# Kernel optimization log

Hardware: AMD Instinct MI355X
Metric: run time of the kernel (lower is better)

Reference implementation:

```python
import jax, jax.numpy as jnp
import numpy as np

B, DIM, H, W = 8, 128, 64, 64
HEADS = 8
NUMS = DIM // HEADS   # 16
OUT = 256

def setup_inputs() -> dict:
    key = jax.random.key(0)
    k1, k2, k3, k4, k5 = jax.random.split(key, 5)
    x = jax.random.normal(k1, (B, DIM, H, W), dtype=jnp.float32)
    # per-group 1x1 conv (num_heads -> 1): weight [nums, heads], bias [nums]
    W1 = jax.random.normal(k2, (NUMS, HEADS), dtype=jnp.float32) * (1.0 / np.sqrt(HEADS))
    b1 = jax.random.normal(k3, (NUMS,), dtype=jnp.float32) * 0.01
    # final 1x1 conv (nums*dim -> out_dim): weight [out, nums*dim], bias [out]
    W2 = jax.random.normal(k4, (OUT, NUMS * DIM), dtype=jnp.float32) * (1.0 / np.sqrt(NUMS * DIM))
    b2 = jax.random.normal(k5, (OUT,), dtype=jnp.float32) * 0.01
    return {"x": x, "W1": W1, "b1": b1, "W2": W2, "b2": b2}

def reference(x, W1, b1, W2, b2):
    B_, C, H_, W_ = x.shape
    # split channels into nums groups of num_heads: [B, nums, heads, H, W]
    xg = x.reshape(B_, NUMS, HEADS, H_, W_)
    # per-group 1x1 conv to 1 channel + ReLU -> attention maps [B, nums, H, W]
    fm = jax.nn.relu(jnp.einsum('bghxy,gh->bgxy', xg, W1) + b1[None, :, None, None])
    # broadcast-multiply each map against full x, concat -> [B, nums*dim, H, W]
    feat = (fm[:, :, None, :, :] * x[:, None, :, :, :]).reshape(B_, NUMS * C, H_, W_)
    # final 1x1 conv -> [B, out_dim, H, W]
    out = jnp.einsum('bcxy,oc->boxy', feat, W2) + b2[None, :, None, None]
    return out
```

## Files before the change

### kernel.cpp

```cpp
#include <hip/hip_runtime.h>

typedef float f32x4 __attribute__((ext_vector_type(4)));
typedef int   i32x4 __attribute__((ext_vector_type(4)));
typedef unsigned int u32;

#define HW_N  4096
#define C_N   128
#define G_N   16
#define K_N   2048
#define O_N   256
#define BN    256

__device__ __forceinline__ u32 pack4(float a, float b, float c, float d, float inv) {
  int q0 = (int)rintf(a * inv), q1 = (int)rintf(b * inv);
  int q2 = (int)rintf(c * inv), q3 = (int)rintf(d * inv);
  return (u32)(q0 & 255) | ((u32)(q1 & 255) << 8) |
         ((u32)(q2 & 255) << 16) | ((u32)(q3 & 255) << 24);
}

__global__ void w2q_k(const float* __restrict__ W2, char* __restrict__ w2q,
                      float* __restrict__ sw) {
  int o = blockIdx.x;
  int l = threadIdx.x;
  const f32x4* rp = reinterpret_cast<const f32x4*>(W2 + (size_t)o * K_N + l * 32);
  float v[32]; float am = 0.f;
#pragma unroll
  for (int q = 0; q < 8; ++q) {
    f32x4 t = rp[q];
#pragma unroll
    for (int j = 0; j < 4; ++j) { v[q * 4 + j] = t[j]; am = fmaxf(am, fabsf(t[j])); }
  }
#pragma unroll
  for (int s = 1; s < 64; s <<= 1) am = fmaxf(am, __shfl_xor(am, s, 64));
  am = fmaxf(am, 1e-30f);
  float inv = 127.0f / am;
  if (l == 0) sw[o] = am / 127.0f;
#pragma unroll
  for (int c = 0; c < 2; ++c) {
    int k0 = l * 32 + c * 16;
    u32 pk[4];
#pragma unroll
    for (int q = 0; q < 4; ++q)
      pk[q] = pack4(v[c * 16 + q * 4 + 0], v[c * 16 + q * 4 + 1],
                    v[c * 16 + q * 4 + 2], v[c * 16 + q * 4 + 3], inv);
    int frag = (o >> 4) * 32 + (k0 >> 7) * 2 + ((k0 >> 6) & 1);
    int lif  = (o & 15) + ((k0 >> 4) & 3) * 16;
    *reinterpret_cast<i32x4*>(w2q + (size_t)frag * 1024 + lif * 16) =
        *reinterpret_cast<i32x4*>(pk);
  }
}

__launch_bounds__(512, 2)
__global__ void ccattn_main_k(const float* __restrict__ x,
                              const float* __restrict__ W1,
                              const float* __restrict__ b1,
                              const char* __restrict__ w2q,
                              const float* __restrict__ sw,
                              const float* __restrict__ b2,
                              float* __restrict__ out) {
  __shared__ char  qxT[BN * 128];
  __shared__ float fmT[G_N][BN];
  __shared__ float sxT[BN];
  __shared__ float lmax[2][BN];

  const int tid = threadIdx.x;
  const int bid = blockIdx.x;
  const int mt  = bid >> 7;
  const int pt  = bid & 127;
  const int b   = pt >> 4;
  const int px0 = (pt & 15) * BN;

  const float* xb = x + (size_t)b * C_N * HW_N + px0;

  const int px    = tid & 255;
  const int chalf = tid >> 8;
  float v[8][8];
  {
    float am = 0.f;
#pragma unroll
    for (int gg = 0; gg < 8; ++gg) {
      const int g  = chalf * 8 + gg;
      const int c0 = g * 8;
      float s = b1[g];
#pragma unroll
      for (int j = 0; j < 8; ++j) {
        float t = xb[(size_t)(c0 + j) * HW_N + px];
        v[gg][j] = t;
        s += t * W1[g * 8 + j];
        am = fmaxf(am, fabsf(t));
      }
      fmT[g][px] = fmaxf(s, 0.0f);
    }
    lmax[chalf][px] = am;
  }
  __syncthreads();

  {
    float amax = fmaxf(fmaxf(lmax[0][px], lmax[1][px]), 1e-30f);
    float inv  = 127.0f / amax;
    if (!chalf) sxT[px] = amax / 127.0f;
#pragma unroll
    for (int gr = 0; gr < 4; ++gr) {
      u32 pk[4];
#pragma unroll
      for (int q = 0; q < 4; ++q) {
        const int gg = gr * 2 + (q >> 1);
        const int j0 = (q & 1) * 4;
        pk[q] = pack4(v[gg][j0], v[gg][j0 + 1], v[gg][j0 + 2], v[gg][j0 + 3], inv);
      }
      int gidx = chalf * 4 + gr;
      int byte = px * 128 + ((gidx ^ (px & 7)) << 4);
      *reinterpret_cast<i32x4*>(qxT + byte) = *reinterpret_cast<i32x4*>(pk);
    }
  }
  __syncthreads();

  const int w  = tid >> 6;
  const int l  = tid & 63;
  const int wm = w & 1;
  const int wn = w >> 1;
  const int lc = l & 15;
  const int lk = l >> 4;

  i32x4 bfr[2][4];
#pragma unroll
  for (int ks2 = 0; ks2 < 2; ++ks2)
#pragma unroll
    for (int nf = 0; nf < 4; ++nf) {
      int p    = wn * 64 + nf * 16 + lc;
      int gidx = ks2 * 4 + lk;
      int byte = p * 128 + ((gidx ^ (p & 7)) << 4);
      bfr[ks2][nf] = *reinterpret_cast<const i32x4*>(qxT + byte);
    }

  f32x4 acc[4][4];
  const f32x4 Z = {0.f, 0.f, 0.f, 0.f};
#pragma unroll
  for (int mf = 0; mf < 4; ++mf)
#pragma unroll
    for (int nf = 0; nf < 4; ++nf) acc[mf][nf] = Z;

  const char* abm = w2q + (size_t)(mt * 8 + wm * 4) * 32768 + l * 16;

  i32x4 A0[8], A1[8];
  float snC[4], snN[4];

#define LDG(dst, g)                                                          \
  {                                                                          \
    _Pragma("unroll")                                                        \
    for (int mf = 0; mf < 4; ++mf) {                                         \
      dst[mf * 2]     = *reinterpret_cast<const i32x4*>(abm + (size_t)mf * 32768 + (g) * 2048);        \
      dst[mf * 2 + 1] = *reinterpret_cast<const i32x4*>(abm + (size_t)mf * 32768 + (g) * 2048 + 1024); \
    }                                                                        \
  }
#define LDSN(dst, g)                                                         \
  {                                                                          \
    _Pragma("unroll")                                                        \
    for (int nf = 0; nf < 4; ++nf) dst[nf] = fmT[g][wn * 64 + nf * 16 + lc]; \
  }
#define COMP(buf, sn)                                                        \
  {                                                                          \
    __builtin_amdgcn_s_setprio(1);                                           \
    _Pragma("unroll")                                                        \
    for (int nf = 0; nf < 4; ++nf) {                                         \
      i32x4 P[4];                                                            \
      _Pragma("unroll")                                                      \
      for (int mf = 0; mf < 4; ++mf)                                         \
        P[mf] = __builtin_amdgcn_mfma_i32_16x16x64_i8(                       \
            buf[mf * 2], bfr[0][nf], (i32x4){0, 0, 0, 0}, 0, 0, 0);          \
      _Pragma("unroll")                                                      \
      for (int mf = 0; mf < 4; ++mf)                                         \
        P[mf] = __builtin_amdgcn_mfma_i32_16x16x64_i8(                       \
            buf[mf * 2 + 1], bfr[1][nf], P[mf], 0, 0, 0);                    \
      _Pragma("unroll")                                                      \
      for (int mf = 0; mf < 4; ++mf) {                                       \
        _Pragma("unroll")                                                    \
        for (int i = 0; i < 4; ++i)                                          \
          acc[mf][nf][i] += sn[nf] * (float)P[mf][i];                        \
      }                                                                      \
    }                                                                        \
    __builtin_amdgcn_s_setprio(0);                                           \
  }

  LDG(A0, 0)
  LDSN(snC, 0)

#pragma unroll 1
  for (int g = 0; g < 16; g += 2) {
    LDG(A1, g + 1)
    LDSN(snN, g + 1)
    COMP(A0, snC)
    const int g2 = (g + 2 < 16) ? g + 2 : 15;
    LDG(A0, g2)
    LDSN(snC, g2)
    COMP(A1, snN)
  }
#undef LDG
#undef LDSN
#undef COMP

  float sxv[4];
#pragma unroll
  for (int nf = 0; nf < 4; ++nf) sxv[nf] = sxT[wn * 64 + nf * 16 + lc];
  float* outb = out + (size_t)b * O_N * HW_N + px0;
#pragma unroll
  for (int mf = 0; mf < 4; ++mf) {
    int o0 = mt * 128 + wm * 64 + mf * 16 + lk * 4;
#pragma unroll
    for (int i = 0; i < 4; ++i) {
      float so   = sw[o0 + i];
      float bias = b2[o0 + i];
#pragma unroll
      for (int nf = 0; nf < 4; ++nf) {
        int p = wn * 64 + nf * 16 + lc;
        outb[(size_t)(o0 + i) * HW_N + p] = acc[mf][nf][i] * so * sxv[nf] + bias;
      }
    }
  }
}

extern "C" void kernel_launch(void* const* d_in, const int* in_sizes, int n_in,
                              void* d_out, int out_size, void* d_ws, size_t ws_size,
                              hipStream_t stream) {
  const float* x  = (const float*)d_in[0];
  const float* W1 = (const float*)d_in[1];
  const float* b1 = (const float*)d_in[2];
  const float* W2 = (const float*)d_in[3];
  const float* b2 = (const float*)d_in[4];
  float* out = (float*)d_out;
  char*  w2q = (char*)d_ws;
  float* sw  = (float*)((char*)d_ws + 524288);

  w2q_k<<<256, 64, 0, stream>>>(W2, w2q, sw);
  ccattn_main_k<<<256, 512, 0, stream>>>(x, W1, b1, w2q, sw, b2, out);
}
```

Before: 40.91 us.

## Keep W2 int8 fragments register-resident and loop over pixel sub-tiles per block

The main kernel becomes 512 blocks of 256 threads. Each wave now holds its full 16-row W2 int8 slice (32 fragments) in registers for the whole block, instead of streaming A fragments from global memory per group. Each block walks four 64-pixel sub-tiles, prefetching the next x sub-tile into registers while the current one is quantized and multiplied, with double-buffered LDS. This cuts repeated W2 global traffic and raises the block count, at the cost of heavy register pressure (128 VGPRs for A alone) and extra barriers per sub-tile.

```diff
diff --git a/kernel.cpp b/kernel.cpp
--- a/kernel.cpp
+++ b/kernel.cpp
@@ -9,7 +9,6 @@
 #define G_N   16
 #define K_N   2048
 #define O_N   256
-#define BN    256
 
 __device__ __forceinline__ u32 pack4(float a, float b, float c, float d, float inv) {
   int q0 = (int)rintf(a * inv), q1 = (int)rintf(b * inv);
@@ -50,7 +49,7 @@
   }
 }
 
-__launch_bounds__(512, 2)
+__launch_bounds__(256, 2)
 __global__ void ccattn_main_k(const float* __restrict__ x,
                               const float* __restrict__ W1,
                               const float* __restrict__ b1,
@@ -58,165 +57,143 @@
                               const float* __restrict__ sw,
                               const float* __restrict__ b2,
                               float* __restrict__ out) {
-  __shared__ char  qxT[BN * 128];
-  __shared__ float fmT[G_N][BN];
-  __shared__ float sxT[BN];
-  __shared__ float lmax[2][BN];
+  __shared__ char  qxT[2][64 * 128];
+  __shared__ float fmT[2][G_N][64];
+  __shared__ float sxT[2][64];
+  __shared__ float lmax[4][64];
 
   const int tid = threadIdx.x;
   const int bid = blockIdx.x;
-  const int mt  = bid >> 7;
-  const int pt  = bid & 127;
-  const int b   = pt >> 4;
-  const int px0 = (pt & 15) * BN;
-
-  const float* xb = x + (size_t)b * C_N * HW_N + px0;
-
-  const int px    = tid & 255;
-  const int chalf = tid >> 8;
-  float v[8][8];
-  {
-    float am = 0.f;
-#pragma unroll
-    for (int gg = 0; gg < 8; ++gg) {
-      const int g  = chalf * 8 + gg;
-      const int c0 = g * 8;
-      float s = b1[g];
-#pragma unroll
-      for (int j = 0; j < 8; ++j) {
-        float t = xb[(size_t)(c0 + j) * HW_N + px];
-        v[gg][j] = t;
-        s += t * W1[g * 8 + j];
-        am = fmaxf(am, fabsf(t));
-      }
-      fmT[g][px] = fmaxf(s, 0.0f);
-    }
-    lmax[chalf][px] = am;
-  }
-  __syncthreads();
-
-  {
-    float amax = fmaxf(fmaxf(lmax[0][px], lmax[1][px]), 1e-30f);
-    float inv  = 127.0f / amax;
-    if (!chalf) sxT[px] = amax / 127.0f;
-#pragma unroll
-    for (int gr = 0; gr < 4; ++gr) {
-      u32 pk[4];
-#pragma unroll
-      for (int q = 0; q < 4; ++q) {
-        const int gg = gr * 2 + (q >> 1);
-        const int j0 = (q & 1) * 4;
-        pk[q] = pack4(v[gg][j0], v[gg][j0 + 1], v[gg][j0 + 2], v[gg][j0 + 3], inv);
-      }
-      int gidx = chalf * 4 + gr;
-      int byte = px * 128 + ((gidx ^ (px & 7)) << 4);
-      *reinterpret_cast<i32x4*>(qxT + byte) = *reinterpret_cast<i32x4*>(pk);
-    }
-  }
-  __syncthreads();
+  const int ot    = bid & 3;
+  const int chunk = bid >> 2;
+  const int b     = chunk >> 4;
+  const int poff  = (chunk & 15) * 256;
 
   const int w  = tid >> 6;
   const int l  = tid & 63;
-  const int wm = w & 1;
-  const int wn = w >> 1;
   const int lc = l & 15;
   const int lk = l >> 4;
-
-  i32x4 bfr[2][4];
-#pragma unroll
-  for (int ks2 = 0; ks2 < 2; ++ks2)
-#pragma unroll
-    for (int nf = 0; nf < 4; ++nf) {
-      int p    = wn * 64 + nf * 16 + lc;
-      int gidx = ks2 * 4 + lk;
-      int byte = p * 128 + ((gidx ^ (p & 7)) << 4);
-      bfr[ks2][nf] = *reinterpret_cast<const i32x4*>(qxT + byte);
+  const int mtile = ot * 4 + w;
+
+  const char* abase = w2q + (size_t)mtile * 32768 + l * 16;
+  i32x4 A[32];
+#pragma unroll
+  for (int f = 0; f < 32; ++f)
+    A[f] = *reinterpret_cast<const i32x4*>(abase + f * 1024);
+
+  const int o0 = mtile * 16 + lk * 4;
+  float swv[4], b2v[4];
+#pragma unroll
+  for (int i = 0; i < 4; ++i) { swv[i] = sw[o0 + i]; b2v[i] = b2[o0 + i]; }
+
+  const int px = tid & 63;
+  const int cq = tid >> 6;
+
+  const float* xb   = x   + (size_t)b * C_N * HW_N + poff;
+  float*       outb = out + (size_t)b * O_N * HW_N + poff;
+
+  float v[4][8];
+#define STLD(pt)                                                    \
+  {                                                                 \
+    const float* xp = xb + (pt) * 64 + px;                          \
+    _Pragma("unroll")                                               \
+    for (int gg = 0; gg < 4; ++gg) {                                \
+      _Pragma("unroll")                                             \
+      for (int j = 0; j < 8; ++j)                                   \
+        v[gg][j] = xp[(size_t)(cq * 32 + gg * 8 + j) * HW_N];       \
+    }                                                               \
+  }
+  STLD(0)
+
+#pragma unroll 1
+  for (int pt = 0; pt < 4; ++pt) {
+    const int tb = pt & 1;
+    {
+      float am = 0.f, s[4];
+#pragma unroll
+      for (int gg = 0; gg < 4; ++gg) {
+        s[gg] = b1[cq * 4 + gg];
+#pragma unroll
+        for (int j = 0; j < 8; ++j) {
+          am = fmaxf(am, fabsf(v[gg][j]));
+          s[gg] += v[gg][j] * W1[(cq * 4 + gg) * 8 + j];
+        }
+      }
+      lmax[cq][px] = am;
+#pragma unroll
+      for (int gg = 0; gg < 4; ++gg) fmT[tb][cq * 4 + gg][px] = fmaxf(s[gg], 0.f);
+      __syncthreads();
+      float amax = fmaxf(fmaxf(fmaxf(lmax[0][px], lmax[1][px]),
+                               fmaxf(lmax[2][px], lmax[3][px])), 1e-30f);
+      float inv = 127.f / amax;
+      if (cq == 0) sxT[tb][px] = amax / 127.f;
+#pragma unroll
+      for (int gr = 0; gr < 2; ++gr) {
+        u32 pk[4];
+#pragma unroll
+        for (int q = 0; q < 4; ++q) {
+          int gg = gr * 2 + (q >> 1);
+          int j0 = (q & 1) * 4;
+          pk[q] = pack4(v[gg][j0], v[gg][j0+1], v[gg][j0+2], v[gg][j0+3], inv);
+        }
+        int gidx = cq * 2 + gr;
+        int byte = px * 128 + ((gidx ^ (px & 7)) << 4);
+        *reinterpret_cast<i32x4*>(&qxT[tb][0] + byte) = *reinterpret_cast<i32x4*>(pk);
+      }
     }
-
-  f32x4 acc[4][4];
-  const f32x4 Z = {0.f, 0.f, 0.f, 0.f};
-#pragma unroll
-  for (int mf = 0; mf < 4; ++mf)
-#pragma unroll
-    for (int nf = 0; nf < 4; ++nf) acc[mf][nf] = Z;
-
-  const char* abm = w2q + (size_t)(mt * 8 + wm * 4) * 32768 + l * 16;
-
-  i32x4 A0[8], A1[8];
-  float snC[4], snN[4];
-
-#define LDG(dst, g)                                                          \
-  {                                                                          \
-    _Pragma("unroll")                                                        \
-    for (int mf = 0; mf < 4; ++mf) {                                         \
-      dst[mf * 2]     = *reinterpret_cast<const i32x4*>(abm + (size_t)mf * 32768 + (g) * 2048);        \
-      dst[mf * 2 + 1] = *reinterpret_cast<const i32x4*>(abm + (size_t)mf * 32768 + (g) * 2048 + 1024); \
-    }                                                                        \
-  }
-#define LDSN(dst, g)                                                         \
-  {                                                                          \
-    _Pragma("unroll")                                                        \
-    for (int nf = 0; nf < 4; ++nf) dst[nf] = fmT[g][wn * 64 + nf * 16 + lc]; \
-  }
-#define COMP(buf, sn)                                                        \
-  {                                                                          \
-    __builtin_amdgcn_s_setprio(1);                                           \
-    _Pragma("unroll")                                                        \
-    for (int nf = 0; nf < 4; ++nf) {                                         \
-      i32x4 P[4];                                                            \
-      _Pragma("unroll")                                                      \
-      for (int mf = 0; mf < 4; ++mf)                                         \
-        P[mf] = __builtin_amdgcn_mfma_i32_16x16x64_i8(                       \
-            buf[mf * 2], bfr[0][nf], (i32x4){0, 0, 0, 0}, 0, 0, 0);          \
-      _Pragma("unroll")                                                      \
-      for (int mf = 0; mf < 4; ++mf)                                         \
-        P[mf] = __builtin_amdgcn_mfma_i32_16x16x64_i8(                       \
-            buf[mf * 2 + 1], bfr[1][nf], P[mf], 0, 0, 0);                    \
-      _Pragma("unroll")                                                      \
-      for (int mf = 0; mf < 4; ++mf) {                                       \
-        _Pragma("unroll")                                                    \
-        for (int i = 0; i < 4; ++i)                                          \
-          acc[mf][nf][i] += sn[nf] * (float)P[mf][i];                        \
-      }                                                                      \
-    }                                                                        \
-    __builtin_amdgcn_s_setprio(0);                                           \
-  }
-
-  LDG(A0, 0)
-  LDSN(snC, 0)
-
-#pragma unroll 1
-  for (int g = 0; g < 16; g += 2) {
-    LDG(A1, g + 1)
-    LDSN(snN, g + 1)
-    COMP(A0, snC)
-    const int g2 = (g + 2 < 16) ? g + 2 : 15;
-    LDG(A0, g2)
-    LDSN(snC, g2)
-    COMP(A1, snN)
-  }
-#undef LDG
-#undef LDSN
-#undef COMP
-
-  float sxv[4];
-#pragma unroll
-  for (int nf = 0; nf < 4; ++nf) sxv[nf] = sxT[wn * 64 + nf * 16 + lc];
-  float* outb = out + (size_t)b * O_N * HW_N + px0;
-#pragma unroll
-  for (int mf = 0; mf < 4; ++mf) {
-    int o0 = mt * 128 + wm * 64 + mf * 16 + lk * 4;
+    __syncthreads();
+    if (pt < 3) STLD(pt + 1)
+
+    i32x4 bfr[2][4];
+#pragma unroll
+    for (int ks2 = 0; ks2 < 2; ++ks2)
+#pragma unroll
+      for (int nf = 0; nf < 4; ++nf) {
+        int p    = nf * 16 + lc;
+        int gidx = ks2 * 4 + lk;
+        int byte = p * 128 + ((gidx ^ (p & 7)) << 4);
+        bfr[ks2][nf] = *reinterpret_cast<const i32x4*>(&qxT[tb][0] + byte);
+      }
+
+    f32x4 acc[4];
+#pragma unroll
+    for (int nf = 0; nf < 4; ++nf) acc[nf] = (f32x4){0.f, 0.f, 0.f, 0.f};
+
+    __builtin_amdgcn_s_setprio(1);
+#pragma unroll
+    for (int g = 0; g < 16; ++g) {
+      i32x4 P[4];
+#pragma unroll
+      for (int nf = 0; nf < 4; ++nf)
+        P[nf] = __builtin_amdgcn_mfma_i32_16x16x64_i8(
+            A[g * 2], bfr[0][nf], (i32x4){0, 0, 0, 0}, 0, 0, 0);
+#pragma unroll
+      for (int nf = 0; nf < 4; ++nf)
+        P[nf] = __builtin_amdgcn_mfma_i32_16x16x64_i8(
+            A[g * 2 + 1], bfr[1][nf], P[nf], 0, 0, 0);
+#pragma unroll
+      for (int nf = 0; nf < 4; ++nf) {
+        float sn = fmT[tb][g][nf * 16 + lc];
+#pragma unroll
+        for (int i = 0; i < 4; ++i)
+          acc[nf][i] += sn * (float)P[nf][i];
+      }
+    }
+    __builtin_amdgcn_s_setprio(0);
+
+    float sxv[4];
+#pragma unroll
+    for (int nf = 0; nf < 4; ++nf) sxv[nf] = sxT[tb][nf * 16 + lc];
 #pragma unroll
     for (int i = 0; i < 4; ++i) {
-      float so   = sw[o0 + i];
-      float bias = b2[o0 + i];
-#pragma unroll
-      for (int nf = 0; nf < 4; ++nf) {
-        int p = wn * 64 + nf * 16 + lc;
-        outb[(size_t)(o0 + i) * HW_N + p] = acc[mf][nf][i] * so * sxv[nf] + bias;
-      }
+#pragma unroll
+      for (int nf = 0; nf < 4; ++nf)
+        outb[(size_t)(o0 + i) * HW_N + pt * 64 + nf * 16 + lc] =
+            acc[nf][i] * swv[i] * sxv[nf] + b2v[i];
     }
-  }
+    __syncthreads();
+  }
+#undef STLD
 }
 
 extern "C" void kernel_launch(void* const* d_in, const int* in_sizes, int n_in,
@@ -232,5 +209,5 @@
   float* sw  = (float*)((char*)d_ws + 524288);
 
   w2q_k<<<256, 64, 0, stream>>>(W2, w2q, sw);
-  ccattn_main_k<<<256, 512, 0, stream>>>(x, W1, b1, w2q, sw, b2, out);
-}
+  ccattn_main_k<<<512, 256, 0, stream>>>(x, W1, b1, w2q, sw, b2, out);
+}
```

After: 49.87 us. 21.9% more time.
